# Kernel optimization log

Measured on AMD Instinct MI355X. Metric: run time of the kernel, lower is better.

The kernel has to match this reference:

```python
import jax, jax.numpy as jnp
import numpy as np

N_USERS = 8192
N_ITEMS = 4096
BATCH = 8192


def setup_inputs() -> dict:
    key = jax.random.key(0)
    k1, k2, k3, k4, k5, k6, k7 = jax.random.split(key, 7)
    # ratings in {0..5}; zeros mark unrated entries (needed for nonzero masking)
    rating_mtx = jax.random.randint(k1, (N_USERS, N_ITEMS), 0, 6).astype(jnp.float32)
    user = jax.random.randint(k2, (BATCH,), 0, N_USERS)
    item = jax.random.randint(k3, (BATCH,), 0, N_ITEMS)
    # learned parameters (xavier-normal similarity; biases initialized like global mean)
    xavier_std = float(np.sqrt(2.0 / (N_USERS + N_USERS)))
    user_similarity = jax.random.normal(k4, (N_USERS, N_USERS), dtype=jnp.float32) * xavier_std
    user_bias = jax.random.normal(k5, (N_USERS,), dtype=jnp.float32)
    item_bias = jax.random.normal(k6, (N_ITEMS,), dtype=jnp.float32)
    global_bias = jax.random.normal(k7, (), dtype=jnp.float32)
    return {
        "user": user,
        "item": item,
        "rating_mtx": rating_mtx,
        "user_similarity": user_similarity,
        "user_bias": user_bias,
        "item_bias": item_bias,
        "global_bias": global_bias,
    }


def reference(user, item, rating_mtx, user_similarity, user_bias, item_bias, global_bias):
    # per-user mean over NONZERO ratings (0 if user rated nothing) -- single fused
    # masked sum/count reduction replacing the per-row python loop
    mask = rating_mtx != 0  # [U, I]
    cnt = jnp.sum(mask, axis=1)  # [U]
    row_sum = jnp.sum(rating_mtx, axis=1)  # zeros contribute nothing
    user_bias_fixed = jnp.where(cnt > 0, row_sum / jnp.maximum(cnt, 1).astype(rating_mtx.dtype), 0.0)

    adjusted = rating_mtx - user_bias_fixed[:, None]  # [U, I]
    similarities = user_similarity[user]  # [B, U]
    item_ratings = adjusted[:, item]  # [U, B]
    user_scores = jnp.sum(similarities * item_ratings.T, axis=1)  # [B]

    bias = user_bias[user] + item_bias[item] + global_bias  # [B]
    return jax.nn.sigmoid(user_scores + bias) * 5.0
```

## Files before the change

### kernel.cpp

```cpp
#include <hip/hip_runtime.h>
#include <math.h>

#define N_USERS 8192
#define N_ITEMS 4096
#define BATCH   8192
#define NTILE_I (N_ITEMS / 64)

__global__ __launch_bounds__(256) void k_trans(const float* __restrict__ R,
                                               unsigned char* __restrict__ AT,
                                               float* __restrict__ psum,
                                               float* __restrict__ pcnt) {
    __shared__ float lds[64][65];
    const int colBase = blockIdx.x * 64;
    const int rowBase = blockIdx.y * 64;
    const int tx = threadIdx.x, ty = threadIdx.y;
    const int x4 = tx * 4;

    float s[4], c[4];
    #pragma unroll
    for (int k = 0; k < 4; ++k) {
        const int y = ty + 16 * k;
        float4 v = *(const float4*)(R + (size_t)(rowBase + y) * N_ITEMS + colBase + x4);
        lds[y][x4 + 0] = v.x;
        lds[y][x4 + 1] = v.y;
        lds[y][x4 + 2] = v.z;
        lds[y][x4 + 3] = v.w;
        s[k] = v.x + v.y + v.z + v.w;
        c[k] = (v.x != 0.f) + (v.y != 0.f) + (v.z != 0.f) + (v.w != 0.f);
    }
    #pragma unroll
    for (int k = 0; k < 4; ++k) {
        #pragma unroll
        for (int off = 8; off; off >>= 1) {
            s[k] += __shfl_down(s[k], off, 16);
            c[k] += __shfl_down(c[k], off, 16);
        }
    }
    if (tx == 0) {
        #pragma unroll
        for (int k = 0; k < 4; ++k) {
            const int u = rowBase + ty + 16 * k;
            psum[(size_t)blockIdx.x * N_USERS + u] = s[k];
            pcnt[(size_t)blockIdx.x * N_USERS + u] = c[k];
        }
    }
    __syncthreads();

    const int tid = ty * 16 + tx;
    #pragma unroll
    for (int ss = 0; ss < 2; ++ss) {
        const int idx = ss * 256 + tid;
        const int il = idx >> 3;
        const int ch = idx & 7;
        unsigned long long w = 0;
        #pragma unroll
        for (int e = 0; e < 8; ++e) {
            w |= (unsigned long long)(unsigned char)(int)lds[ch * 8 + e][il] << (8 * e);
        }
        *(unsigned long long*)(AT + (size_t)(colBase + il) * N_USERS + rowBase + ch * 8) = w;
    }
}

__global__ __launch_bounds__(256) void k_fin(const float* __restrict__ psum,
                                             const float* __restrict__ pcnt,
                                             float* __restrict__ ub) {
    const int u = blockIdx.x * 256 + threadIdx.x;
    float s = 0.f, c = 0.f;
    #pragma unroll
    for (int t = 0; t < NTILE_I; ++t) {
        s += psum[(size_t)t * N_USERS + u];
        c += pcnt[(size_t)t * N_USERS + u];
    }
    ub[u] = (c > 0.f) ? s / fmaxf(c, 1.f) : 0.f;
}

__global__ __launch_bounds__(256) void k_main(const float* __restrict__ S,
                                              const unsigned char* __restrict__ AT,
                                              const float* __restrict__ ub,
                                              const int* __restrict__ user,
                                              const int* __restrict__ item,
                                              const float* __restrict__ ubias,
                                              const float* __restrict__ ibias,
                                              const float* __restrict__ gbias,
                                              float* __restrict__ out) {
    const int wave = threadIdx.x >> 6;
    const int lane = threadIdx.x & 63;
    const int b = blockIdx.x * 4 + wave;
    const int su = user[b];
    const int j  = item[b];
    const float4* srow  = (const float4*)(S + (size_t)su * N_USERS);
    const float4* ubrow = (const float4*)ub;
    const uint2*  arow  = (const uint2*)(AT + (size_t)j * N_USERS);

    float acc = 0.f;
    #pragma unroll 4
    for (int i = 0; i < 16; ++i) {
        const int idx = i * 64 + lane;
        uint2  a  = arow[idx];
        float4 s0 = srow[2 * idx + 0];
        float4 s1 = srow[2 * idx + 1];
        float4 u0 = ubrow[2 * idx + 0];
        float4 u1 = ubrow[2 * idx + 1];
        acc += s0.x * ((float)( a.x        & 0xffu) - u0.x);
        acc += s0.y * ((float)((a.x >>  8) & 0xffu) - u0.y);
        acc += s0.z * ((float)((a.x >> 16) & 0xffu) - u0.z);
        acc += s0.w * ((float)( a.x >> 24         ) - u0.w);
        acc += s1.x * ((float)( a.y        & 0xffu) - u1.x);
        acc += s1.y * ((float)((a.y >>  8) & 0xffu) - u1.y);
        acc += s1.z * ((float)((a.y >> 16) & 0xffu) - u1.z);
        acc += s1.w * ((float)( a.y >> 24         ) - u1.w);
    }
    #pragma unroll
    for (int off = 32; off; off >>= 1) acc += __shfl_down(acc, off);

    if (lane == 0) {
        float score = acc + ubias[su] + ibias[j] + gbias[0];
        out[b] = 5.f / (1.f + expf(-score));
    }
}

__global__ __launch_bounds__(256) void k_ubfix(const float* __restrict__ R,
                                               float* __restrict__ ub) {
    const int wave = threadIdx.x >> 6;
    const int lane = threadIdx.x & 63;
    const int u = blockIdx.x * 4 + wave;
    const float4* row4 = (const float4*)(R + (size_t)u * N_ITEMS);
    float s = 0.f, c = 0.f;
    #pragma unroll
    for (int i = 0; i < 16; ++i) {
        float4 v = row4[i * 64 + lane];
        s += v.x + v.y + v.z + v.w;
        c += (v.x != 0.f) + (v.y != 0.f) + (v.z != 0.f) + (v.w != 0.f);
    }
    #pragma unroll
    for (int off = 32; off; off >>= 1) {
        s += __shfl_down(s, off);
        c += __shfl_down(c, off);
    }
    if (lane == 0)
        ub[u] = (c > 0.f) ? s / fmaxf(c, 1.f) : 0.f;
}

__global__ __launch_bounds__(256) void k_direct(const float* __restrict__ S,
                                                const float* __restrict__ R,
                                                const float* __restrict__ ub,
                                                const int* __restrict__ user,
                                                const int* __restrict__ item,
                                                const float* __restrict__ ubias,
                                                const float* __restrict__ ibias,
                                                const float* __restrict__ gbias,
                                                float* __restrict__ out) {
    const int b = blockIdx.x;
    const int su = user[b];
    const int j  = item[b];
    const float* srow = S + (size_t)su * N_USERS;
    float acc = 0.f;
    for (int u = threadIdx.x; u < N_USERS; u += 256) {
        acc += srow[u] * (R[(size_t)u * N_ITEMS + j] - ub[u]);
    }
    for (int off = 32; off; off >>= 1) acc += __shfl_down(acc, off);
    __shared__ float sa[4];
    const int lane = threadIdx.x & 63, w = threadIdx.x >> 6;
    if (lane == 0) sa[w] = acc;
    __syncthreads();
    if (threadIdx.x == 0) {
        float score = sa[0] + sa[1] + sa[2] + sa[3]
                    + ubias[su] + ibias[j] + gbias[0];
        out[b] = 5.f / (1.f + expf(-score));
    }
}

extern "C" void kernel_launch(void* const* d_in, const int* in_sizes, int n_in,
                              void* d_out, int out_size, void* d_ws, size_t ws_size,
                              hipStream_t stream) {
    const int*   user  = (const int*)d_in[0];
    const int*   item  = (const int*)d_in[1];
    const float* R     = (const float*)d_in[2];
    const float* S     = (const float*)d_in[3];
    const float* ubias = (const float*)d_in[4];
    const float* ibias = (const float*)d_in[5];
    const float* gbias = (const float*)d_in[6];
    float* out = (float*)d_out;

    float* ub   = (float*)d_ws;
    float* psum = (float*)((char*)d_ws + (64u << 10));
    float* pcnt = (float*)((char*)d_ws + (64u << 10) + ((size_t)NTILE_I * N_USERS * 4));
    unsigned char* AT = (unsigned char*)((char*)d_ws + (8u << 20));
    const size_t need = (8u << 20) + (size_t)N_ITEMS * N_USERS;

    if (ws_size >= need) {
        dim3 tgrid(NTILE_I, N_USERS / 64);
        dim3 tblk(16, 16);
        k_trans<<<tgrid, tblk, 0, stream>>>(R, AT, psum, pcnt);
        k_fin<<<N_USERS / 256, 256, 0, stream>>>(psum, pcnt, ub);
        k_main<<<BATCH / 4, 256, 0, stream>>>(S, AT, ub, user, item, ubias, ibias, gbias, out);
    } else {
        k_ubfix<<<N_USERS / 4, 256, 0, stream>>>(R, ub);
        k_direct<<<BATCH, 256, 0, stream>>>(S, R, ub, user, item, ubias, ibias, gbias, out);
    }
}
```

Measured before the change: 477.1 us.

## Widen transpose stores, split k_fin reduction, stage user means in LDS

The transpose kernel now writes each transposed byte row chunk as a single 16-byte store instead of two 8-byte stores per thread. The mean-finalize kernel splits the 64 partial tiles across four waves and reduces them through shared memory, which launches more blocks and exposes more parallelism. The main kernel uses 512-thread blocks and loads the 32KB user-mean vector into LDS once per block rather than reading it from global or L2 in every wave. These changes cut global traffic and raise memory-level parallelism, at the cost of a block-wide sync and higher LDS use that may limit occupancy.

```diff
diff --git a/kernel.cpp b/kernel.cpp
--- a/kernel.cpp
+++ b/kernel.cpp
@@ -47,50 +47,63 @@
     __syncthreads();
 
     const int tid = ty * 16 + tx;
-    #pragma unroll
-    for (int ss = 0; ss < 2; ++ss) {
-        const int idx = ss * 256 + tid;
-        const int il = idx >> 3;
-        const int ch = idx & 7;
-        unsigned long long w = 0;
-        #pragma unroll
-        for (int e = 0; e < 8; ++e) {
-            w |= (unsigned long long)(unsigned char)(int)lds[ch * 8 + e][il] << (8 * e);
-        }
-        *(unsigned long long*)(AT + (size_t)(colBase + il) * N_USERS + rowBase + ch * 8) = w;
-    }
+    const int il = tid >> 2;
+    const int ch = tid & 3;
+    union { unsigned char b[16]; int4 v; } w;
+    #pragma unroll
+    for (int e = 0; e < 16; ++e) {
+        w.b[e] = (unsigned char)(int)lds[ch * 16 + e][il];
+    }
+    *(int4*)(AT + (size_t)(colBase + il) * N_USERS + rowBase + ch * 16) = w.v;
 }
 
 __global__ __launch_bounds__(256) void k_fin(const float* __restrict__ psum,
                                              const float* __restrict__ pcnt,
                                              float* __restrict__ ub) {
-    const int u = blockIdx.x * 256 + threadIdx.x;
+    __shared__ float ss[4][64], sc[4][64];
+    const int ul  = threadIdx.x & 63;
+    const int seg = threadIdx.x >> 6;
+    const int u = blockIdx.x * 64 + ul;
     float s = 0.f, c = 0.f;
     #pragma unroll
-    for (int t = 0; t < NTILE_I; ++t) {
+    for (int k = 0; k < 16; ++k) {
+        const int t = seg * 16 + k;
         s += psum[(size_t)t * N_USERS + u];
         c += pcnt[(size_t)t * N_USERS + u];
     }
-    ub[u] = (c > 0.f) ? s / fmaxf(c, 1.f) : 0.f;
-}
-
-__global__ __launch_bounds__(256) void k_main(const float* __restrict__ S,
-                                              const unsigned char* __restrict__ AT,
-                                              const float* __restrict__ ub,
-                                              const int* __restrict__ user,
-                                              const int* __restrict__ item,
-                                              const float* __restrict__ ubias,
-                                              const float* __restrict__ ibias,
-                                              const float* __restrict__ gbias,
-                                              float* __restrict__ out) {
+    ss[seg][ul] = s;
+    sc[seg][ul] = c;
+    __syncthreads();
+    if (seg == 0) {
+        s = ss[0][ul] + ss[1][ul] + ss[2][ul] + ss[3][ul];
+        c = sc[0][ul] + sc[1][ul] + sc[2][ul] + sc[3][ul];
+        ub[u] = (c > 0.f) ? s / fmaxf(c, 1.f) : 0.f;
+    }
+}
+
+__global__ __launch_bounds__(512, 6) void k_main(const float* __restrict__ S,
+                                                 const unsigned char* __restrict__ AT,
+                                                 const float* __restrict__ ub,
+                                                 const int* __restrict__ user,
+                                                 const int* __restrict__ item,
+                                                 const float* __restrict__ ubias,
+                                                 const float* __restrict__ ibias,
+                                                 const float* __restrict__ gbias,
+                                                 float* __restrict__ out) {
+    __shared__ float4 ubs[N_USERS / 4];
+    #pragma unroll
+    for (int t = 0; t < 4; ++t) {
+        ubs[t * 512 + threadIdx.x] = ((const float4*)ub)[t * 512 + threadIdx.x];
+    }
+    __syncthreads();
+
     const int wave = threadIdx.x >> 6;
     const int lane = threadIdx.x & 63;
-    const int b = blockIdx.x * 4 + wave;
+    const int b = blockIdx.x * 8 + wave;
     const int su = user[b];
     const int j  = item[b];
-    const float4* srow  = (const float4*)(S + (size_t)su * N_USERS);
-    const float4* ubrow = (const float4*)ub;
-    const uint2*  arow  = (const uint2*)(AT + (size_t)j * N_USERS);
+    const float4* srow = (const float4*)(S + (size_t)su * N_USERS);
+    const uint2*  arow = (const uint2*)(AT + (size_t)j * N_USERS);
 
     float acc = 0.f;
     #pragma unroll 4
@@ -99,8 +112,8 @@
         uint2  a  = arow[idx];
         float4 s0 = srow[2 * idx + 0];
         float4 s1 = srow[2 * idx + 1];
-        float4 u0 = ubrow[2 * idx + 0];
-        float4 u1 = ubrow[2 * idx + 1];
+        float4 u0 = ubs[2 * idx + 0];
+        float4 u1 = ubs[2 * idx + 1];
         acc += s0.x * ((float)( a.x        & 0xffu) - u0.x);
         acc += s0.y * ((float)((a.x >>  8) & 0xffu) - u0.y);
         acc += s0.z * ((float)((a.x >> 16) & 0xffu) - u0.z);
@@ -192,8 +205,8 @@
         dim3 tgrid(NTILE_I, N_USERS / 64);
         dim3 tblk(16, 16);
         k_trans<<<tgrid, tblk, 0, stream>>>(R, AT, psum, pcnt);
-        k_fin<<<N_USERS / 256, 256, 0, stream>>>(psum, pcnt, ub);
-        k_main<<<BATCH / 4, 256, 0, stream>>>(S, AT, ub, user, item, ubias, ibias, gbias, out);
+        k_fin<<<N_USERS / 64, 256, 0, stream>>>(psum, pcnt, ub);
+        k_main<<<BATCH / 8, 512, 0, stream>>>(S, AT, ub, user, item, ubias, ibias, gbias, out);
     } else {
         k_ubfix<<<N_USERS / 4, 256, 0, stream>>>(R, ub);
         k_direct<<<BATCH, 256, 0, stream>>>(S, R, ub, user, item, ubias, ibias, gbias, out);
```

Result: faster. 442.9 us, median of 2 (-7.2%).
